# Performance work log

Hardware: AMD Instinct MI355X
Metric: run time of the kernel (lower is better)

## Reference

```python
import jax, jax.numpy as jnp
import numpy as np

EPS = 1e-5

def layernorm2d(x, w, b):
    # nn.LayerNorm([T, C]): normalize jointly over last two dims, affine shape [T, C]
    mu = jnp.mean(x, axis=(-2, -1), keepdims=True)
    var = jnp.mean(jnp.square(x - mu), axis=(-2, -1), keepdims=True)
    return (x - mu) * jax.lax.rsqrt(var + EPS) * w + b


def setup_inputs() -> dict:
    key = jax.random.key(0)
    ks = jax.random.split(key, 10)
    B, T, C = 64, 512, 512
    s = 0.02
    inputs = jax.random.normal(ks[0], (B, T, C), dtype=jnp.float32)
    ln1_w = jnp.ones((T, C), dtype=jnp.float32)
    ln1_b = jnp.zeros((T, C), dtype=jnp.float32)
    ln2_w = jnp.ones((T, C), dtype=jnp.float32)
    ln2_b = jnp.zeros((T, C), dtype=jnp.float32)
    # TriU: row i holds the Linear(i+1,1) weights for prefix 0..i -> lower-triangular [T,T]
    tri_M = jax.random.normal(ks[1], (T, T), dtype=jnp.float32) * s
    tri_b = jax.random.normal(ks[2], (T,), dtype=jnp.float32) * s
    d1_w = jax.random.normal(ks[3], (C, C), dtype=jnp.float32) * s  # dense_1: out = x @ d1_w.T + d1_b
    d1_b = jax.random.normal(ks[4], (C,), dtype=jnp.float32) * s
    d2_w = jax.random.normal(ks[5], (C, C), dtype=jnp.float32) * s
    d2_b = jax.random.normal(ks[6], (C,), dtype=jnp.float32) * s
    return {"inputs": inputs, "ln1_w": ln1_w, "ln1_b": ln1_b,
            "ln2_w": ln2_w, "ln2_b": ln2_b,
            "tri_M": tri_M, "tri_b": tri_b,
            "d1_w": d1_w, "d1_b": d1_b, "d2_w": d2_w, "d2_b": d2_b}


def reference(inputs, ln1_w, ln1_b, ln2_w, ln2_b, tri_M, tri_b, d1_w, d1_b, d2_w, d2_b):
    # x: [B, T, C]
    x = layernorm2d(inputs, ln1_w, ln1_b)
    # TriU time mixer: out[b,i,c] = sum_{j<=i} M[i,j] * x[b,j,c] + tri_b[i]
    M = jnp.tril(tri_M)
    x = jnp.einsum('it,btc->bic', M, x) + tri_b[None, :, None]
    x = layernorm2d(x + inputs, ln2_w, ln2_b)
    # channel mixer MLP (dropout = 0)
    h = jax.nn.gelu(jnp.einsum('btc,hc->bth', x, d1_w) + d1_b, approximate=False)
    y = jnp.einsum('bth,ch->btc', h, d2_w) + d2_b
    return x + y
```

## Files before the change

### kernel.cpp

```cpp
#include <hip/hip_runtime.h>
#include <hip/hip_bf16.h>
#include <math.h>


#define B_ 64
#define T_ 512
#define C_ 512
#define TC_ (T_ * C_)
static_assert(TC_ == 262144, "");

typedef __attribute__((ext_vector_type(8))) short bf16x8;
typedef __attribute__((ext_vector_type(4))) float f32x4;

__device__ __forceinline__ unsigned short f2bf(float f) {
  union { float f; unsigned u; } v; v.f = f;
  unsigned r = v.u + 0x7FFF + ((v.u >> 16) & 1);
  return (unsigned short)(r >> 16);
}
__device__ __forceinline__ float bf2f(unsigned short h) {
  union { unsigned u; float f; } v; v.u = ((unsigned)h) << 16; return v.f;
}

__device__ __forceinline__ void load16_lds(const void* gsrc, void* ldst) {
  __builtin_amdgcn_global_load_lds(
      (const __attribute__((address_space(1))) unsigned int*)gsrc,
      (__attribute__((address_space(3))) unsigned int*)ldst,
      16, 0, 0);
}

__global__ __launch_bounds__(256) void conv_weights(
    const float* __restrict__ triM, const float* __restrict__ d1w,
    const float* __restrict__ d2w, unsigned short* __restrict__ Mb,
    unsigned short* __restrict__ W1b, unsigned short* __restrict__ W2b) {
  const int idx = blockIdx.x * 256 + threadIdx.x;
  const int i = idx >> 9, j = idx & 511;
  Mb[idx]  = (j <= i) ? f2bf(triM[idx]) : (unsigned short)0;
  W1b[idx] = f2bf(d1w[idx]);
  W2b[idx] = f2bf(d2w[idx]);
}

__global__ __launch_bounds__(256) void ln_stats(const float* __restrict__ x,
                                                float* __restrict__ red) {
  const int b = blockIdx.x;
  const int s = blockIdx.y;
  const float4* p = (const float4*)(x + (size_t)b * TC_) + (size_t)s * 4096;
  float s1 = 0.f, s2 = 0.f;
  for (int i = threadIdx.x; i < 4096; i += 256) {
    float4 v = p[i];
    s1 += v.x + v.y + v.z + v.w;
    s2 += v.x * v.x + v.y * v.y + v.z * v.z + v.w * v.w;
  }
#pragma unroll
  for (int o = 32; o; o >>= 1) { s1 += __shfl_down(s1, o, 64); s2 += __shfl_down(s2, o, 64); }
  __shared__ float sm[8];
  const int w = threadIdx.x >> 6, lane = threadIdx.x & 63;
  if (lane == 0) { sm[w * 2] = s1; sm[w * 2 + 1] = s2; }
  __syncthreads();
  if (threadIdx.x == 0) {
    float a = 0.f, c = 0.f;
    for (int i = 0; i < 4; ++i) { a += sm[2 * i]; c += sm[2 * i + 1]; }
    atomicAdd(&red[b * 2], a);
    atomicAdd(&red[b * 2 + 1], c);
  }
}

__global__ __launch_bounds__(256) void ln1_norm_t(
    const float* __restrict__ x, const float* __restrict__ w,
    const float* __restrict__ bvec, const float* __restrict__ red1,
    unsigned short* __restrict__ XnT) {
  __shared__ unsigned short tile[64][65];
  const int b = blockIdx.z;
  const int t0 = blockIdx.y * 64;
  const int c0 = blockIdx.x * 64;
  const float mu = red1[b * 2] * (1.f / TC_);
  const float rstd = rsqrtf(red1[b * 2 + 1] * (1.f / TC_) - mu * mu + 1e-5f);
  const int tid = threadIdx.x;
  const int r = tid >> 4;
  const int cg = (tid & 15) * 4;
#pragma unroll
  for (int rr = 0; rr < 4; ++rr) {
    const int t = t0 + rr * 16 + r;
    const float4 xv = *(const float4*)&x[((size_t)b * T_ + t) * C_ + c0 + cg];
    const float4 wv = *(const float4*)&w[(size_t)t * C_ + c0 + cg];
    const float4 bv = *(const float4*)&bvec[(size_t)t * C_ + c0 + cg];
    tile[rr * 16 + r][cg + 0] = f2bf((xv.x - mu) * rstd * wv.x + bv.x);
    tile[rr * 16 + r][cg + 1] = f2bf((xv.y - mu) * rstd * wv.y + bv.y);
    tile[rr * 16 + r][cg + 2] = f2bf((xv.z - mu) * rstd * wv.z + bv.z);
    tile[rr * 16 + r][cg + 3] = f2bf((xv.w - mu) * rstd * wv.w + bv.w);
  }
  __syncthreads();
  const int cl = tid >> 2;
  const int tg = (tid & 3) * 16;
  alignas(16) unsigned short tmp[16];
#pragma unroll
  for (int j = 0; j < 16; ++j) tmp[j] = tile[tg + j][cl];
  unsigned short* o = &XnT[((size_t)b * C_ + c0 + cl) * T_ + t0 + tg];
  *(uint4*)&o[0] = *(const uint4*)&tmp[0];
  *(uint4*)&o[8] = *(const uint4*)&tmp[8];
}

__device__ __forceinline__ void stage_tile256(
    const unsigned short* __restrict__ Ag, const unsigned short* __restrict__ Bg,
    int k0, unsigned short* As, unsigned short* Bs, int tid) {
#pragma unroll
  for (int j = 0; j < 2; ++j) {
    const int c = tid + 512 * j;
    const int row = c >> 2;
    const int l = (c & 3) ^ ((row ^ (row >> 2)) & 3);
    load16_lds(Ag + ((size_t)row << 9) + k0 + l * 8, As + c * 8);
  }
#pragma unroll
  for (int j = 0; j < 2; ++j) {
    const int c = tid + 512 * j;
    const int row = c >> 2;
    const int l = (c & 3) ^ ((row ^ (row >> 2)) & 3);
    load16_lds(Bg + ((size_t)row << 9) + k0 + l * 8, Bs + c * 8);
  }
}

__device__ __forceinline__ void mfma_tile(
    const unsigned short* __restrict__ Ac, const unsigned short* __restrict__ Bc,
    int arow, int brow, int co, f32x4 acc[8][4]) {
  bf16x8 af[8], bfr[4];
#pragma unroll
  for (int m = 0; m < 8; ++m)
    af[m] = *(const bf16x8*)&Ac[arow + m * 512 + co];
#pragma unroll
  for (int n = 0; n < 4; ++n)
    bfr[n] = *(const bf16x8*)&Bc[brow + n * 512 + co];
  __builtin_amdgcn_s_setprio(1);
#pragma unroll
  for (int m = 0; m < 8; ++m)
#pragma unroll
    for (int n = 0; n < 4; ++n)
      acc[m][n] = __builtin_amdgcn_mfma_f32_16x16x32_bf16(af[m], bfr[n], acc[m][n], 0, 0, 0);
  __builtin_amdgcn_s_setprio(0);
}

__device__ __forceinline__ void gemm_mainloop256(
    const unsigned short* __restrict__ Ag, const unsigned short* __restrict__ Bg,
    int ktiles,
    unsigned short* lds, f32x4 acc[8][4], int tid) {
  const int lane = tid & 63, w = tid >> 6;
  const int wm = w >> 2, wn = w & 3;
  const int m16 = lane & 15, quad = lane >> 4;
  unsigned short* A0 = lds;
  unsigned short* B0 = lds + 8192;
  unsigned short* A1 = lds + 16384;
  unsigned short* B1 = lds + 24576;
  const int arow = (wm * 128 + m16) * 32;
  const int brow = (wn * 64 + m16) * 32;
  const int co = ((quad ^ ((m16 ^ (m16 >> 2)) & 3)) * 8);
  stage_tile256(Ag, Bg, 0, A0, B0, tid);
  __syncthreads();
  for (int kt = 0; kt < ktiles; kt += 2) {
    stage_tile256(Ag, Bg, (kt + 1) * 32, A1, B1, tid);
    mfma_tile(A0, B0, arow, brow, co, acc);
    __syncthreads();
    if (kt + 2 < ktiles)
      stage_tile256(Ag, Bg, (kt + 2) * 32, A0, B0, tid);
    mfma_tile(A1, B1, arow, brow, co, acc);
    __syncthreads();
  }
}

__device__ __forceinline__ int xcd_swizzle_256(int bid) {
  return ((bid & 7) << 5) | (bid >> 3);
}

__global__ __launch_bounds__(512, 2) void gemm_mixer(
    const unsigned short* __restrict__ Mb, const unsigned short* __restrict__ XnT,
    const float* __restrict__ trib, const float* __restrict__ inp,
    unsigned short* __restrict__ Z, float* __restrict__ red2) {
  __shared__ __align__(16) unsigned short lds[32768];
  const int swz = xcd_swizzle_256((int)blockIdx.x);
  const int b = swz >> 2;
  const int i0 = ((swz >> 1) & 1) * 256;
  const int c0 = (swz & 1) * 256;
  f32x4 acc[8][4];
#pragma unroll
  for (int m = 0; m < 8; ++m)
#pragma unroll
    for (int n = 0; n < 4; ++n) acc[m][n] = (f32x4){0.f, 0.f, 0.f, 0.f};
  gemm_mainloop256(Mb + (size_t)i0 * T_, XnT + (size_t)b * TC_ + (size_t)c0 * T_,
                   (i0 + 256) >> 5, lds, acc, (int)threadIdx.x);
  const int tid = threadIdx.x, lane = tid & 63, w = tid >> 6;
  const int wm = w >> 2, wn = w & 3, m16 = lane & 15, quad = lane >> 4;
  const int rbase = i0 + wm * 128, cbase = c0 + wn * 64;
  float s1 = 0.f, s2 = 0.f;
#pragma unroll
  for (int m = 0; m < 8; ++m) {
#pragma unroll
    for (int g = 0; g < 4; ++g) {
      const int i = rbase + m * 16 + quad * 4 + g;
      const float tb = trib[i];
      const float* inrow = &inp[((size_t)b * T_ + i) * C_];
      unsigned short* zrow = &Z[((size_t)b * T_ + i) * C_];
#pragma unroll
      for (int n = 0; n < 4; ++n) {
        const int ch = cbase + n * 16 + m16;
        const float v = acc[m][n][g] + tb + inrow[ch];
        zrow[ch] = f2bf(v);
        s1 += v; s2 += v * v;
      }
    }
  }
#pragma unroll
  for (int o = 32; o; o >>= 1) { s1 += __shfl_down(s1, o, 64); s2 += __shfl_down(s2, o, 64); }
  float* smf = (float*)lds;
  if (lane == 0) { smf[w * 2] = s1; smf[w * 2 + 1] = s2; }
  __syncthreads();
  if (tid == 0) {
    float a = 0.f, c2 = 0.f;
    for (int i = 0; i < 8; ++i) { a += smf[2 * i]; c2 += smf[2 * i + 1]; }
    atomicAdd(&red2[b * 2], a);
    atomicAdd(&red2[b * 2 + 1], c2);
  }
}

__global__ __launch_bounds__(256) void ln2_norm(
    const unsigned short* __restrict__ Z, const float* __restrict__ red2,
    const float* __restrict__ w, const float* __restrict__ bvec,
    unsigned short* __restrict__ X2) {
  const size_t e = ((size_t)blockIdx.x * 256 + threadIdx.x) * 8;
  const int b = (int)(e >> 18);
  const int tc = (int)(e & (TC_ - 1));
  const float mu = red2[b * 2] * (1.f / TC_);
  const float rstd = rsqrtf(red2[b * 2 + 1] * (1.f / TC_) - mu * mu + 1e-5f);
  uint4 zp = *(const uint4*)&Z[e];
  const unsigned short* zs = (const unsigned short*)&zp;
  alignas(16) float wv[8], bb[8];
  *(float4*)&wv[0] = *(const float4*)&w[tc];
  *(float4*)&wv[4] = *(const float4*)&w[tc + 4];
  *(float4*)&bb[0] = *(const float4*)&bvec[tc];
  *(float4*)&bb[4] = *(const float4*)&bvec[tc + 4];
  alignas(16) unsigned short o[8];
#pragma unroll
  for (int j = 0; j < 8; ++j)
    o[j] = f2bf((bf2f(zs[j]) - mu) * rstd * wv[j] + bb[j]);
  *(uint4*)&X2[e] = *(const uint4*)&o[0];
}

__global__ __launch_bounds__(512, 2) void gemm_d1(
    const unsigned short* __restrict__ X2, const unsigned short* __restrict__ W1b,
    const float* __restrict__ d1b, unsigned short* __restrict__ H) {
  __shared__ __align__(16) unsigned short lds[32768];
  const int swz = xcd_swizzle_256((int)blockIdx.x);
  const int n0 = (swz >> 7) * 256;
  const int i0 = (swz & 127) * 256;
  f32x4 acc[8][4];
#pragma unroll
  for (int m = 0; m < 8; ++m)
#pragma unroll
    for (int n = 0; n < 4; ++n) acc[m][n] = (f32x4){0.f, 0.f, 0.f, 0.f};
  gemm_mainloop256(X2 + (size_t)i0 * C_, W1b + (size_t)n0 * C_, 16, lds, acc,
                   (int)threadIdx.x);
  const int tid = threadIdx.x, lane = tid & 63, w = tid >> 6;
  const int wm = w >> 2, wn = w & 3, m16 = lane & 15, quad = lane >> 4;
  const int rbase = i0 + wm * 128, cbase = n0 + wn * 64;
#pragma unroll
  for (int m = 0; m < 8; ++m) {
#pragma unroll
    for (int g = 0; g < 4; ++g) {
      const int row = rbase + m * 16 + quad * 4 + g;
#pragma unroll
      for (int n = 0; n < 4; ++n) {
        const int col = cbase + n * 16 + m16;
        const float v = acc[m][n][g] + d1b[col];
        const float gl = 0.5f * v * (1.0f + erff(v * 0.70710678118654752f));
        H[(size_t)row * C_ + col] = f2bf(gl);
      }
    }
  }
}

__global__ __launch_bounds__(512, 2) void gemm_d2(
    const unsigned short* __restrict__ H, const unsigned short* __restrict__ W2b,
    const float* __restrict__ d2b, const unsigned short* __restrict__ X2,
    float* __restrict__ out) {
  __shared__ __align__(16) unsigned short lds[32768];
  const int swz = xcd_swizzle_256((int)blockIdx.x);
  const int n0 = (swz >> 7) * 256;
  const int i0 = (swz & 127) * 256;
  f32x4 acc[8][4];
#pragma unroll
  for (int m = 0; m < 8; ++m)
#pragma unroll
    for (int n = 0; n < 4; ++n) acc[m][n] = (f32x4){0.f, 0.f, 0.f, 0.f};
  gemm_mainloop256(H + (size_t)i0 * C_, W2b + (size_t)n0 * C_, 16, lds, acc,
                   (int)threadIdx.x);
  const int tid = threadIdx.x, lane = tid & 63, w = tid >> 6;
  const int wm = w >> 2, wn = w & 3, m16 = lane & 15, quad = lane >> 4;
  const int rbase = i0 + wm * 128, cbase = n0 + wn * 64;
#pragma unroll
  for (int m = 0; m < 8; ++m) {
#pragma unroll
    for (int g = 0; g < 4; ++g) {
      const int row = rbase + m * 16 + quad * 4 + g;
#pragma unroll
      for (int n = 0; n < 4; ++n) {
        const int col = cbase + n * 16 + m16;
        out[(size_t)row * C_ + col] =
            acc[m][n][g] + d2b[col] + bf2f(X2[(size_t)row * C_ + col]);
      }
    }
  }
}

extern "C" void kernel_launch(void* const* d_in, const int* in_sizes, int n_in,
                              void* d_out, int out_size, void* d_ws, size_t ws_size,
                              hipStream_t stream) {
  const float* inp  = (const float*)d_in[0];
  const float* ln1w = (const float*)d_in[1];
  const float* ln1b = (const float*)d_in[2];
  const float* ln2w = (const float*)d_in[3];
  const float* ln2b = (const float*)d_in[4];
  const float* triM = (const float*)d_in[5];
  const float* trib = (const float*)d_in[6];
  const float* d1w  = (const float*)d_in[7];
  const float* d1b  = (const float*)d_in[8];
  const float* d2w  = (const float*)d_in[9];
  const float* d2b  = (const float*)d_in[10];
  float* out = (float*)d_out;

  char* ws = (char*)d_ws;
  float* red1 = (float*)ws;
  float* red2 = (float*)(ws + 512);
  unsigned short* Mb  = (unsigned short*)(ws + 1024);
  unsigned short* W1b = Mb + TC_;
  unsigned short* W2b = W1b + TC_;
  unsigned short* XnT = W2b + TC_;
  unsigned short* Z   = XnT + (size_t)B_ * TC_;
  unsigned short* X2  = Z + (size_t)B_ * TC_;
  unsigned short* H   = X2 + (size_t)B_ * TC_;

  hipMemsetAsync(ws, 0, 1024, stream);
  conv_weights<<<1024, 256, 0, stream>>>(triM, d1w, d2w, Mb, W1b, W2b);
  ln_stats<<<dim3(B_, 16), 256, 0, stream>>>(inp, red1);
  ln1_norm_t<<<dim3(8, 8, B_), 256, 0, stream>>>(inp, ln1w, ln1b, red1, XnT);
  gemm_mixer<<<256, 512, 0, stream>>>(Mb, XnT, trib, inp, Z, red2);
  ln2_norm<<<8192, 256, 0, stream>>>(Z, red2, ln2w, ln2b, X2);
  gemm_d1<<<256, 512, 0, stream>>>(X2, W1b, d1b, H);
  gemm_d2<<<256, 512, 0, stream>>>(H, W2b, d2b, X2, out);
}
```

Measured before the change: 270.8 us.

## Use single-buffered K=64 GEMM tiles with register prefetch; merge prep kernels

The shared GEMM main loop moves from double-buffered K=32 LDS tiles filled by direct global-to-LDS loads to a single K=64 LDS buffer. The next tile is prefetched into registers and written to LDS after a barrier, with a new XOR swizzle over 8 chunks. This halves the number of barrier pairs per K and gives more MFMA work per iteration, at the cost of extra registers and an explicit LDS store phase. The weight-conversion and LN1-statistics kernels are also merged into one launch to save a kernel dispatch.

```diff
diff --git a/kernel.cpp b/kernel.cpp
--- a/kernel.cpp
+++ b/kernel.cpp
@@ -28,21 +28,22 @@
       16, 0, 0);
 }
 
-__global__ __launch_bounds__(256) void conv_weights(
+__global__ __launch_bounds__(256) void prep(
     const float* __restrict__ triM, const float* __restrict__ d1w,
     const float* __restrict__ d2w, unsigned short* __restrict__ Mb,
-    unsigned short* __restrict__ W1b, unsigned short* __restrict__ W2b) {
-  const int idx = blockIdx.x * 256 + threadIdx.x;
-  const int i = idx >> 9, j = idx & 511;
-  Mb[idx]  = (j <= i) ? f2bf(triM[idx]) : (unsigned short)0;
-  W1b[idx] = f2bf(d1w[idx]);
-  W2b[idx] = f2bf(d2w[idx]);
-}
-
-__global__ __launch_bounds__(256) void ln_stats(const float* __restrict__ x,
-                                                float* __restrict__ red) {
-  const int b = blockIdx.x;
-  const int s = blockIdx.y;
+    unsigned short* __restrict__ W1b, unsigned short* __restrict__ W2b,
+    const float* __restrict__ x, float* __restrict__ red) {
+  if (blockIdx.x < 1024) {
+    const int idx = blockIdx.x * 256 + threadIdx.x;
+    const int i = idx >> 9, j = idx & 511;
+    Mb[idx]  = (j <= i) ? f2bf(triM[idx]) : (unsigned short)0;
+    W1b[idx] = f2bf(d1w[idx]);
+    W2b[idx] = f2bf(d2w[idx]);
+    return;
+  }
+  const int bb = blockIdx.x - 1024;
+  const int b = bb >> 4;
+  const int s = bb & 15;
   const float4* p = (const float4*)(x + (size_t)b * TC_) + (size_t)s * 4096;
   float s1 = 0.f, s2 = 0.f;
   for (int i = threadIdx.x; i < 4096; i += 256) {
@@ -99,67 +100,66 @@
   *(uint4*)&o[8] = *(const uint4*)&tmp[8];
 }
 
-__device__ __forceinline__ void stage_tile256(
-    const unsigned short* __restrict__ Ag, const unsigned short* __restrict__ Bg,
-    int k0, unsigned short* As, unsigned short* Bs, int tid) {
-#pragma unroll
-  for (int j = 0; j < 2; ++j) {
-    const int c = tid + 512 * j;
-    const int row = c >> 2;
-    const int l = (c & 3) ^ ((row ^ (row >> 2)) & 3);
-    load16_lds(Ag + ((size_t)row << 9) + k0 + l * 8, As + c * 8);
-  }
-#pragma unroll
-  for (int j = 0; j < 2; ++j) {
-    const int c = tid + 512 * j;
-    const int row = c >> 2;
-    const int l = (c & 3) ^ ((row ^ (row >> 2)) & 3);
-    load16_lds(Bg + ((size_t)row << 9) + k0 + l * 8, Bs + c * 8);
-  }
-}
-
-__device__ __forceinline__ void mfma_tile(
-    const unsigned short* __restrict__ Ac, const unsigned short* __restrict__ Bc,
-    int arow, int brow, int co, f32x4 acc[8][4]) {
-  bf16x8 af[8], bfr[4];
-#pragma unroll
-  for (int m = 0; m < 8; ++m)
-    af[m] = *(const bf16x8*)&Ac[arow + m * 512 + co];
-#pragma unroll
-  for (int n = 0; n < 4; ++n)
-    bfr[n] = *(const bf16x8*)&Bc[brow + n * 512 + co];
-  __builtin_amdgcn_s_setprio(1);
-#pragma unroll
-  for (int m = 0; m < 8; ++m)
-#pragma unroll
-    for (int n = 0; n < 4; ++n)
-      acc[m][n] = __builtin_amdgcn_mfma_f32_16x16x32_bf16(af[m], bfr[n], acc[m][n], 0, 0, 0);
-  __builtin_amdgcn_s_setprio(0);
-}
-
 __device__ __forceinline__ void gemm_mainloop256(
     const unsigned short* __restrict__ Ag, const unsigned short* __restrict__ Bg,
-    int ktiles,
-    unsigned short* lds, f32x4 acc[8][4], int tid) {
+    int ktiles, unsigned short* As, unsigned short* Bs, f32x4 acc[8][4], int tid) {
   const int lane = tid & 63, w = tid >> 6;
   const int wm = w >> 2, wn = w & 3;
   const int m16 = lane & 15, quad = lane >> 4;
-  unsigned short* A0 = lds;
-  unsigned short* B0 = lds + 8192;
-  unsigned short* A1 = lds + 16384;
-  unsigned short* B1 = lds + 24576;
-  const int arow = (wm * 128 + m16) * 32;
-  const int brow = (wn * 64 + m16) * 32;
-  const int co = ((quad ^ ((m16 ^ (m16 >> 2)) & 3)) * 8);
-  stage_tile256(Ag, Bg, 0, A0, B0, tid);
+  const int arow = (wm * 128 + m16) * 64;
+  const int brow = (wn * 64 + m16) * 64;
+  const int xk = m16 & 7;
+  int rowc[4], lc[4];
+#pragma unroll
+  for (int j = 0; j < 4; ++j) {
+    const int c = tid + 512 * j;
+    rowc[j] = c >> 3;
+    lc[j] = ((c & 7) ^ (rowc[j] & 7)) * 8;
+  }
+#pragma unroll
+  for (int j = 0; j < 4; ++j) {
+    const int c = tid + 512 * j;
+    load16_lds(Ag + ((size_t)rowc[j] << 9) + lc[j], As + c * 8);
+    load16_lds(Bg + ((size_t)rowc[j] << 9) + lc[j], Bs + c * 8);
+  }
   __syncthreads();
-  for (int kt = 0; kt < ktiles; kt += 2) {
-    stage_tile256(Ag, Bg, (kt + 1) * 32, A1, B1, tid);
-    mfma_tile(A0, B0, arow, brow, co, acc);
+  uint4 rA[4], rB[4];
+  for (int T = 0; T < ktiles; ++T) {
+    const int k1 = (T + 1) * 64;
+    if (T + 1 < ktiles) {
+#pragma unroll
+      for (int j = 0; j < 4; ++j) {
+        rA[j] = *(const uint4*)(Ag + ((size_t)rowc[j] << 9) + k1 + lc[j]);
+        rB[j] = *(const uint4*)(Bg + ((size_t)rowc[j] << 9) + k1 + lc[j]);
+      }
+    }
+#pragma unroll
+    for (int ks = 0; ks < 2; ++ks) {
+      const int co = (((ks * 4 + quad) ^ xk) * 8);
+      bf16x8 af[8], bfr[4];
+#pragma unroll
+      for (int m = 0; m < 8; ++m)
+        af[m] = *(const bf16x8*)&As[arow + m * 1024 + co];
+#pragma unroll
+      for (int n = 0; n < 4; ++n)
+        bfr[n] = *(const bf16x8*)&Bs[brow + n * 1024 + co];
+      __builtin_amdgcn_s_setprio(1);
+#pragma unroll
+      for (int m = 0; m < 8; ++m)
+#pragma unroll
+        for (int n = 0; n < 4; ++n)
+          acc[m][n] = __builtin_amdgcn_mfma_f32_16x16x32_bf16(af[m], bfr[n], acc[m][n], 0, 0, 0);
+      __builtin_amdgcn_s_setprio(0);
+    }
     __syncthreads();
-    if (kt + 2 < ktiles)
-      stage_tile256(Ag, Bg, (kt + 2) * 32, A0, B0, tid);
-    mfma_tile(A1, B1, arow, brow, co, acc);
+    if (T + 1 < ktiles) {
+#pragma unroll
+      for (int j = 0; j < 4; ++j) {
+        const int c = tid + 512 * j;
+        *(uint4*)(As + c * 8) = rA[j];
+        *(uint4*)(Bs + c * 8) = rB[j];
+      }
+    }
     __syncthreads();
   }
 }
@@ -183,7 +183,7 @@
 #pragma unroll
     for (int n = 0; n < 4; ++n) acc[m][n] = (f32x4){0.f, 0.f, 0.f, 0.f};
   gemm_mainloop256(Mb + (size_t)i0 * T_, XnT + (size_t)b * TC_ + (size_t)c0 * T_,
-                   (i0 + 256) >> 5, lds, acc, (int)threadIdx.x);
+                   (i0 + 256) >> 6, lds, lds + 16384, acc, (int)threadIdx.x);
   const int tid = threadIdx.x, lane = tid & 63, w = tid >> 6;
   const int wm = w >> 2, wn = w & 3, m16 = lane & 15, quad = lane >> 4;
   const int rbase = i0 + wm * 128, cbase = c0 + wn * 64;
@@ -253,8 +253,8 @@
   for (int m = 0; m < 8; ++m)
 #pragma unroll
     for (int n = 0; n < 4; ++n) acc[m][n] = (f32x4){0.f, 0.f, 0.f, 0.f};
-  gemm_mainloop256(X2 + (size_t)i0 * C_, W1b + (size_t)n0 * C_, 16, lds, acc,
-                   (int)threadIdx.x);
+  gemm_mainloop256(X2 + (size_t)i0 * C_, W1b + (size_t)n0 * C_, 8, lds, lds + 16384,
+                   acc, (int)threadIdx.x);
   const int tid = threadIdx.x, lane = tid & 63, w = tid >> 6;
   const int wm = w >> 2, wn = w & 3, m16 = lane & 15, quad = lane >> 4;
   const int rbase = i0 + wm * 128, cbase = n0 + wn * 64;
@@ -287,8 +287,8 @@
   for (int m = 0; m < 8; ++m)
 #pragma unroll
     for (int n = 0; n < 4; ++n) acc[m][n] = (f32x4){0.f, 0.f, 0.f, 0.f};
-  gemm_mainloop256(H + (size_t)i0 * C_, W2b + (size_t)n0 * C_, 16, lds, acc,
-                   (int)threadIdx.x);
+  gemm_mainloop256(H + (size_t)i0 * C_, W2b + (size_t)n0 * C_, 8, lds, lds + 16384,
+                   acc, (int)threadIdx.x);
   const int tid = threadIdx.x, lane = tid & 63, w = tid >> 6;
   const int wm = w >> 2, wn = w & 3, m16 = lane & 15, quad = lane >> 4;
   const int rbase = i0 + wm * 128, cbase = n0 + wn * 64;
@@ -335,8 +335,7 @@
   unsigned short* H   = X2 + (size_t)B_ * TC_;
 
   hipMemsetAsync(ws, 0, 1024, stream);
-  conv_weights<<<1024, 256, 0, stream>>>(triM, d1w, d2w, Mb, W1b, W2b);
-  ln_stats<<<dim3(B_, 16), 256, 0, stream>>>(inp, red1);
+  prep<<<2048, 256, 0, stream>>>(triM, d1w, d2w, Mb, W1b, W2b, inp, red1);
   ln1_norm_t<<<dim3(8, 8, B_), 256, 0, stream>>>(inp, ln1w, ln1b, red1, XnT);
   gemm_mixer<<<256, 512, 0, stream>>>(Mb, XnT, trib, inp, Z, red2);
   ln2_norm<<<8192, 256, 0, stream>>>(Z, red2, ln2w, ln2b, X2);
```

After: 341.2 us. +26.0%, slower.
